# Performance work log

Hardware: AMD Instinct MI355X
Metric: run time of the kernel (lower is better)

The kernel has to match this reference:

```python
import jax, jax.numpy as jnp
import numpy as np

N_NODES = 50000
N_EDGES = 600000
D_IN = 128
D_HID = 128
D_OUT = 47
BN_EPS = 1e-5


def setup_inputs() -> dict:
    key = jax.random.key(0)
    ks = jax.random.split(key, 16)
    x = jax.random.normal(ks[0], (N_NODES, D_IN), dtype=jnp.float32)
    edge_index = jax.random.randint(ks[1], (2, N_EDGES), 0, N_NODES, dtype=jnp.int64)
    s = 0.05
    return {
        'x': x,
        'edge_index': edge_index,
        # SAGEConv layer 1: lin_l (neighbor agg, with bias), lin_r (root, no bias)
        'W1l': jax.random.normal(ks[2], (D_IN, D_HID), jnp.float32) * s,
        'b1': jnp.zeros((D_HID,), jnp.float32),
        'W1r': jax.random.normal(ks[3], (D_IN, D_HID), jnp.float32) * s,
        # layer 2
        'W2l': jax.random.normal(ks[4], (D_HID, D_HID), jnp.float32) * s,
        'b2': jnp.zeros((D_HID,), jnp.float32),
        'W2r': jax.random.normal(ks[5], (D_HID, D_HID), jnp.float32) * s,
        # layer 3
        'W3l': jax.random.normal(ks[6], (D_HID, D_OUT), jnp.float32) * s,
        'b3': jnp.zeros((D_OUT,), jnp.float32),
        'W3r': jax.random.normal(ks[7], (D_HID, D_OUT), jnp.float32) * s,
        # BatchNorm params (eval mode: running stats)
        'g1': jnp.ones((D_HID,), jnp.float32),
        'be1': jnp.zeros((D_HID,), jnp.float32),
        'm1': jax.random.normal(ks[8], (D_HID,), jnp.float32) * 0.1,
        'v1': jnp.ones((D_HID,), jnp.float32) + jax.random.uniform(ks[9], (D_HID,)) * 0.1,
        'g2': jnp.ones((D_HID,), jnp.float32),
        'be2': jnp.zeros((D_HID,), jnp.float32),
        'm2': jax.random.normal(ks[10], (D_HID,), jnp.float32) * 0.1,
        'v2': jnp.ones((D_HID,), jnp.float32) + jax.random.uniform(ks[11], (D_HID,)) * 0.1,
    }


def _sage_conv(x, src, dst, Wl, b, Wr):
    # mean aggregation of source features at destination nodes
    n = x.shape[0]
    msg = x[src]  # [E, d] gather
    agg = jax.ops.segment_sum(msg, dst, num_segments=n)
    cnt = jax.ops.segment_sum(jnp.ones((src.shape[0],), x.dtype), dst, num_segments=n)
    agg = agg / jnp.maximum(cnt, 1.0)[:, None]  # zero in-degree -> 0
    return agg @ Wl + b + x @ Wr


def _bn_eval(x, g, be, m, v):
    return (x - m) * (g * jax.lax.rsqrt(v + BN_EPS)) + be


def reference(x, edge_index, W1l, b1, W1r, W2l, b2, W2r, W3l, b3, W3r,
              g1, be1, m1, v1, g2, be2, m2, v2):
    src, dst = edge_index[0], edge_index[1]
    h = _sage_conv(x, src, dst, W1l, b1, W1r)
    h = jax.nn.relu(_bn_eval(h, g1, be1, m1, v1))  # dropout is identity in eval
    h = _sage_conv(h, src, dst, W2l, b2, W2r)
    h = jax.nn.relu(_bn_eval(h, g2, be2, m2, v2))
    return _sage_conv(h, src, dst, W3l, b3, W3r)
```

## Files before the change

### kernel.cpp

```cpp
#include <hip/hip_runtime.h>

#define NN 50000
#define NE 600000
#define D 128
#define DOUT3 47
#define ZW 64
#define BN_EPS 1e-5f
#define NPB 256
#define SB 196

typedef __attribute__((ext_vector_type(8))) short short8;
typedef __attribute__((ext_vector_type(4))) float f32x4;

__device__ inline unsigned short f2b(float f) {
  union { float f; unsigned u; } c; c.f = f;
  unsigned u = c.u;
  unsigned r = (u + 0x7FFFu + ((u >> 16) & 1u)) >> 16;
  return (unsigned short)r;
}
__device__ inline float b2f(unsigned short h) {
  union { unsigned u; float f; } c; c.u = ((unsigned)h) << 16;
  return c.f;
}

__global__ void zero_int(int* __restrict__ p, int n) {
  int i = blockIdx.x * blockDim.x + threadIdx.x;
  if (i < n) p[i] = 0;
}

__global__ __launch_bounds__(256) void prep_hist(
    const float4* __restrict__ x4, unsigned short* __restrict__ xb,
    const float* __restrict__ W1l, const float* __restrict__ W1r, unsigned short* __restrict__ Bt1,
    const float* __restrict__ W2l, const float* __restrict__ W2r, unsigned short* __restrict__ Bt2,
    const float* __restrict__ W3l, const float* __restrict__ W3r, unsigned short* __restrict__ Bt3,
    const int* __restrict__ dst, int* __restrict__ deg) {
  int b = blockIdx.x;
  int t = threadIdx.x;
  if (b < 1024) {
    long n4 = (long)NN * D / 4;
    for (long i = (long)b * 256 + t; i < n4; i += 1024L * 256) {
      float4 v = x4[i];
      uint2 p;
      p.x = (unsigned)f2b(v.x) | ((unsigned)f2b(v.y) << 16);
      p.y = (unsigned)f2b(v.z) | ((unsigned)f2b(v.w) << 16);
      *(uint2*)(xb + i * 4) = p;
    }
  } else if (b < 1280) {
    const float* Wl = (b < 1152) ? W1l : W2l;
    const float* Wr = (b < 1152) ? W1r : W2r;
    unsigned short* Bt = (b < 1152) ? Bt1 : Bt2;
    int idx = ((b < 1152) ? (b - 1024) : (b - 1152)) * 256 + t;
    int j = idx >> 8, k = idx & 255;
    float v = (k < 128) ? Wl[k * D + j] : Wr[(k - 128) * D + j];
    Bt[idx] = f2b(v);
  } else if (b < 1336) {
    int idx = (b - 1280) * 256 + t;
    if (idx < 112 * 128) {
      int j = idx >> 7, k = idx & 127;
      float v = 0.f;
      if (j < DOUT3) v = W3l[k * DOUT3 + j];
      else if (j >= 64 && j < 64 + DOUT3) v = W3r[k * DOUT3 + (j - 64)];
      Bt3[idx] = f2b(v);
    }
  } else {
    int e = (b - 1336) * 256 + t;
    if (e < NE) {
      int d = dst[e];
      d = max(0, min(NN - 1, d));
      atomicAdd(&deg[d], 1);
    }
  }
}

__global__ __launch_bounds__(NPB) void scan_local(const int* __restrict__ deg,
                                                  int* __restrict__ row_start,
                                                  int* __restrict__ partials) {
  __shared__ int s[NPB];
  int t = threadIdx.x;
  int i = blockIdx.x * NPB + t;
  int v = (i < NN) ? deg[i] : 0;
  s[t] = v;
  __syncthreads();
  for (int off = 1; off < NPB; off <<= 1) {
    int u = (t >= off) ? s[t - off] : 0;
    __syncthreads();
    s[t] += u;
    __syncthreads();
  }
  if (i < NN) row_start[i] = s[t] - v;
  if (t == NPB - 1) partials[blockIdx.x] = s[NPB - 1];
}

__global__ __launch_bounds__(NPB) void scan_add(int* __restrict__ row_start,
                                                const int* __restrict__ partials,
                                                int* __restrict__ cursor) {
  __shared__ int s[NPB];
  int t = threadIdx.x;
  int v = (t < SB) ? partials[t] : 0;
  s[t] = v;
  __syncthreads();
  for (int off = 1; off < NPB; off <<= 1) {
    int u = (t >= off) ? s[t - off] : 0;
    __syncthreads();
    s[t] += u;
    __syncthreads();
  }
  int base = s[blockIdx.x] - partials[blockIdx.x];
  int i = blockIdx.x * NPB + t;
  if (i < NN) {
    int r = row_start[i] + base;
    row_start[i] = r;
    cursor[i] = r;
  }
  if (i == 0) row_start[NN] = NE;
}

__global__ void build_kernel(const int* __restrict__ src, const int* __restrict__ dst,
                             int* __restrict__ cursor, int* __restrict__ srcs, int E) {
  int e = blockIdx.x * blockDim.x + threadIdx.x;
  if (e < E) {
    int d = dst[e];
    d = max(0, min(NN - 1, d));
    int s = src[e];
    s = max(0, min(NN - 1, s));
    int pos = atomicAdd(&cursor[d], 1);
    srcs[pos] = s;
  }
}

__global__ __launch_bounds__(256) void fused_gather_mfma(
    const unsigned short* __restrict__ feat,
    const int* __restrict__ row_start, const int* __restrict__ srcs,
    const unsigned short* __restrict__ Bt, const float* __restrict__ bias,
    const float* __restrict__ g, const float* __restrict__ be,
    const float* __restrict__ m, const float* __restrict__ v,
    unsigned short* __restrict__ outb) {
  __shared__ __align__(16) unsigned short s_a[16][136];
  int tid = threadIdx.x;
  int row0 = blockIdx.x * 16;
  int grp = tid >> 4, s = tid & 15;
  const unsigned short* fp = feat + s * 8;

  {
    int node = row0 + grp;
    int start = row_start[node], end = row_start[node + 1];
    float a[8];
#pragma unroll
    for (int i = 0; i < 8; i++) a[i] = 0.f;
    for (int base = start; base < end; base += 16) {
      int cnt = min(end - base, 16);
      int idxv = (base + s < end) ? srcs[base + s] : 0;
      int M = (cnt + 3) >> 2;
      for (int q = 0; q < M; q++) {
        int e0 = q * 4;
        int s0 = __shfl(idxv, e0 + 0, 16);
        int s1 = __shfl(idxv, e0 + 1, 16);
        int s2 = __shfl(idxv, e0 + 2, 16);
        int s3 = __shfl(idxv, e0 + 3, 16);
        float w1 = (e0 + 1 < cnt) ? 1.f : 0.f;
        float w2 = (e0 + 2 < cnt) ? 1.f : 0.f;
        float w3 = (e0 + 3 < cnt) ? 1.f : 0.f;
        short8 v0 = *(const short8*)(fp + (long)s0 * D);
        short8 v1 = *(const short8*)(fp + (long)s1 * D);
        short8 v2 = *(const short8*)(fp + (long)s2 * D);
        short8 v3 = *(const short8*)(fp + (long)s3 * D);
#pragma unroll
        for (int i = 0; i < 8; i++)
          a[i] += (b2f((unsigned short)v0[i]) + w1 * b2f((unsigned short)v1[i])) +
                  (w2 * b2f((unsigned short)v2[i]) + w3 * b2f((unsigned short)v3[i]));
      }
    }
    float iv = 1.0f / fmaxf((float)(end - start), 1.0f);
    uint4 p;
    p.x = (unsigned)f2b(a[0] * iv) | ((unsigned)f2b(a[1] * iv) << 16);
    p.y = (unsigned)f2b(a[2] * iv) | ((unsigned)f2b(a[3] * iv) << 16);
    p.z = (unsigned)f2b(a[4] * iv) | ((unsigned)f2b(a[5] * iv) << 16);
    p.w = (unsigned)f2b(a[6] * iv) | ((unsigned)f2b(a[7] * iv) << 16);
    *(uint4*)&s_a[grp][s * 8] = p;
  }

  __syncthreads();

  int lane = tid & 63, wid = tid >> 6;
  int r15 = lane & 15, hi = lane >> 4;
  f32x4 acc[2];
  acc[0] = (f32x4)(0.f);
  acc[1] = (f32x4)(0.f);

  const unsigned short* As = &s_a[r15][hi * 8];
  const unsigned short* Ax = feat + (long)(row0 + r15) * D + hi * 8;
  const unsigned short* Bp = Bt + (long)(wid * 2) * 16 * 256 + (long)r15 * 256 + hi * 8;

#pragma unroll
  for (int kf = 0; kf < 8; kf++) {
    const int kk = kf * 32;
    short8 a = (kf < 4) ? *(const short8*)(As + kk)
                        : *(const short8*)(Ax + (kk - 128));
#pragma unroll
    for (int f = 0; f < 2; f++) {
      short8 b = *(const short8*)(Bp + (long)f * 16 * 256 + kk);
      acc[f] = __builtin_amdgcn_mfma_f32_16x16x32_bf16(a, b, acc[f], 0, 0, 0);
    }
  }

#pragma unroll
  for (int f = 0; f < 2; f++) {
    int col = wid * 32 + f * 16 + r15;
    float bj = bias[col];
    float sc = g[col] * rsqrtf(v[col] + BN_EPS);
    float sh = be[col] - m[col] * sc;
#pragma unroll
    for (int r = 0; r < 4; r++) {
      int row = row0 + hi * 4 + r;
      float val = fmaxf((acc[f][r] + bj) * sc + sh, 0.f);
      outb[(long)row * D + col] = f2b(val);
    }
  }
}

__global__ __launch_bounds__(256) void trans_mfma(
    const unsigned short* __restrict__ xb, const unsigned short* __restrict__ Bt3,
    const float* __restrict__ bias, unsigned short* __restrict__ Z,
    float* __restrict__ outP, int tiles) {
  const int NF = 7;
  int wid = threadIdx.x >> 6, lane = threadIdx.x & 63;
  int tile = blockIdx.x * 4 + wid;
  if (tile >= tiles) return;
  int row0 = tile * 16;
  int r15 = lane & 15, hi = lane >> 4;

  f32x4 acc[NF];
#pragma unroll
  for (int f = 0; f < NF; f++) acc[f] = (f32x4)(0.f);

  const unsigned short* Ar = xb + (long)(row0 + r15) * D + hi * 8;
  const unsigned short* Bp = Bt3 + (long)r15 * 128 + hi * 8;

#pragma unroll
  for (int kf = 0; kf < 4; kf++) {
    const int kk = kf * 32;
    short8 a = *(const short8*)(Ar + kk);
#pragma unroll
    for (int f = 0; f < NF; f++) {
      short8 b = *(const short8*)(Bp + (long)f * 16 * 128 + kk);
      acc[f] = __builtin_amdgcn_mfma_f32_16x16x32_bf16(a, b, acc[f], 0, 0, 0);
    }
  }

#pragma unroll
  for (int f = 0; f < NF; f++) {
    int col = f * 16 + r15;
#pragma unroll
    for (int r = 0; r < 4; r++) {
      int row = row0 + hi * 4 + r;
      float val = acc[f][r];
      if (col < ZW) {
        Z[(long)row * ZW + col] = f2b(val);
      } else {
        int pc = col - 64;
        if (pc < DOUT3) outP[(long)row * DOUT3 + pc] = val + bias[pc];
      }
    }
  }
}

__global__ __launch_bounds__(256) void gather_add47(const unsigned short* __restrict__ Z,
                                                    const int* __restrict__ row_start,
                                                    const int* __restrict__ srcs,
                                                    float* __restrict__ outP) {
  int t = blockIdx.x * blockDim.x + threadIdx.x;
  int node = t >> 4;
  int s = t & 15;
  if (node >= NN) return;
  int start = row_start[node], end = row_start[node + 1];
  float a[4];
#pragma unroll
  for (int i = 0; i < 4; i++) a[i] = 0.f;
  const unsigned short* zp = Z + s * 4;
  for (int base = start; base < end; base += 16) {
    int cnt = min(end - base, 16);
    int idxv = (base + s < end) ? srcs[base + s] : 0;
    int M = (cnt + 3) >> 2;
    for (int q = 0; q < M; q++) {
      int e0 = q * 4;
      int s0 = __shfl(idxv, e0 + 0, 16);
      int s1 = __shfl(idxv, e0 + 1, 16);
      int s2 = __shfl(idxv, e0 + 2, 16);
      int s3 = __shfl(idxv, e0 + 3, 16);
      float w1 = (e0 + 1 < cnt) ? 1.f : 0.f;
      float w2 = (e0 + 2 < cnt) ? 1.f : 0.f;
      float w3 = (e0 + 3 < cnt) ? 1.f : 0.f;
      uint2 u0 = *(const uint2*)(zp + (long)s0 * ZW);
      uint2 u1 = *(const uint2*)(zp + (long)s1 * ZW);
      uint2 u2 = *(const uint2*)(zp + (long)s2 * ZW);
      uint2 u3 = *(const uint2*)(zp + (long)s3 * ZW);
      a[0] += (b2f((unsigned short)u0.x) + w1 * b2f((unsigned short)u1.x)) +
              (w2 * b2f((unsigned short)u2.x) + w3 * b2f((unsigned short)u3.x));
      a[1] += (b2f((unsigned short)(u0.x >> 16)) + w1 * b2f((unsigned short)(u1.x >> 16))) +
              (w2 * b2f((unsigned short)(u2.x >> 16)) + w3 * b2f((unsigned short)(u3.x >> 16)));
      a[2] += (b2f((unsigned short)u0.y) + w1 * b2f((unsigned short)u1.y)) +
              (w2 * b2f((unsigned short)u2.y) + w3 * b2f((unsigned short)u3.y));
      a[3] += (b2f((unsigned short)(u0.y >> 16)) + w1 * b2f((unsigned short)(u1.y >> 16))) +
              (w2 * b2f((unsigned short)(u2.y >> 16)) + w3 * b2f((unsigned short)(u3.y >> 16)));
    }
  }
  float iv = 1.0f / fmaxf((float)(end - start), 1.0f);
#pragma unroll
  for (int i = 0; i < 4; i++) {
    int c = s * 4 + i;
    if (c < DOUT3) {
      long o = (long)node * DOUT3 + c;
      outP[o] = outP[o] + a[i] * iv;
    }
  }
}

extern "C" void kernel_launch(void* const* d_in, const int* in_sizes, int n_in,
                              void* d_out, int out_size, void* d_ws, size_t ws_size,
                              hipStream_t stream) {
  const float* x = (const float*)d_in[0];
  const int* ei = (const int*)d_in[1];
  const int* src = ei;
  const int* dst = ei + NE;
  const float* W1l = (const float*)d_in[2];
  const float* b1  = (const float*)d_in[3];
  const float* W1r = (const float*)d_in[4];
  const float* W2l = (const float*)d_in[5];
  const float* b2  = (const float*)d_in[6];
  const float* W2r = (const float*)d_in[7];
  const float* W3l = (const float*)d_in[8];
  const float* b3  = (const float*)d_in[9];
  const float* W3r = (const float*)d_in[10];
  const float* g1  = (const float*)d_in[11];
  const float* be1 = (const float*)d_in[12];
  const float* m1  = (const float*)d_in[13];
  const float* v1  = (const float*)d_in[14];
  const float* g2  = (const float*)d_in[15];
  const float* be2 = (const float*)d_in[16];
  const float* m2  = (const float*)d_in[17];
  const float* v2  = (const float*)d_in[18];

  float* out = (float*)d_out;

  int* deg       = (int*)d_ws;
  int* row_start = deg + NN;
  int* cursor    = row_start + NN + 4;
  int* partials  = cursor + NN;
  int* srcs      = partials + 256;
  unsigned short* xb   = (unsigned short*)(srcs + NE);
  unsigned short* h2b  = xb + (long)NN * D;
  unsigned short* h1b  = h2b + (long)NN * D;
  unsigned short* Zb   = h1b + (long)NN * D;
  unsigned short* Bt1  = Zb + (long)NN * ZW;
  unsigned short* Bt2  = Bt1 + 128 * 256;
  unsigned short* Bt3  = Bt2 + 128 * 256;

  zero_int<<<SB, 256, 0, stream>>>(deg, NN);
  prep_hist<<<3680, 256, 0, stream>>>(
      (const float4*)x, xb, W1l, W1r, Bt1, W2l, W2r, Bt2, W3l, W3r, Bt3, dst, deg);

  scan_local<<<SB, NPB, 0, stream>>>(deg, row_start, partials);
  scan_add<<<SB, NPB, 0, stream>>>(row_start, partials, cursor);
  build_kernel<<<(NE + 255) / 256, 256, 0, stream>>>(src, dst, cursor, srcs, NE);

  int tiles = NN / 16;

  fused_gather_mfma<<<tiles, 256, 0, stream>>>(
      xb, row_start, srcs, Bt1, b1, g1, be1, m1, v1, h1b);

  fused_gather_mfma<<<tiles, 256, 0, stream>>>(
      h1b, row_start, srcs, Bt2, b2, g2, be2, m2, v2, h2b);

  trans_mfma<<<(tiles + 3) / 4, 256, 0, stream>>>(h2b, Bt3, b3, Zb, out, tiles);
  gather_add47<<<(NN * 16 + 255) / 256, 256, 0, stream>>>(Zb, row_start, srcs, out);
}
```

Before: 220.6 us.

## Fuse layer-3 transform into layer-2 kernel and unroll gathers to 8 edges

The layer-3 projection (trans_mfma) is folded into the layer-2 gather+MFMA kernel. The layer-2 activations stay in shared memory and are multiplied by Bt3 there, so h2 is never written to or read back from global memory and one launch is removed. Separately, the neighbor gathers in both the fused kernel and gather_add47 now load source indices directly, clamped to the last edge, and process 8 edges per iteration instead of shuffling 4 at a time. This gives more loads in flight per iteration, at the cost of higher register pressure and redundant index loads, since every lane in a group reads the same indices.

```diff
diff --git a/kernel.cpp b/kernel.cpp
--- a/kernel.cpp
+++ b/kernel.cpp
@@ -128,14 +128,20 @@
   }
 }
 
-__global__ __launch_bounds__(256) void fused_gather_mfma(
+template <bool TR>
+__global__ __launch_bounds__(256) void fused_layer(
     const unsigned short* __restrict__ feat,
     const int* __restrict__ row_start, const int* __restrict__ srcs,
     const unsigned short* __restrict__ Bt, const float* __restrict__ bias,
     const float* __restrict__ g, const float* __restrict__ be,
     const float* __restrict__ m, const float* __restrict__ v,
-    unsigned short* __restrict__ outb) {
+    unsigned short* __restrict__ outb,
+    const unsigned short* __restrict__ Bt3,
+    const float* __restrict__ b3,
+    unsigned short* __restrict__ Z,
+    float* __restrict__ outP) {
   __shared__ __align__(16) unsigned short s_a[16][136];
+  __shared__ __align__(16) unsigned short s_h[TR ? 16 : 1][136];
   int tid = threadIdx.x;
   int row0 = blockIdx.x * 16;
   int grp = tid >> 4, s = tid & 15;
@@ -144,30 +150,41 @@
   {
     int node = row0 + grp;
     int start = row_start[node], end = row_start[node + 1];
+    int last = end - 1;
     float a[8];
 #pragma unroll
     for (int i = 0; i < 8; i++) a[i] = 0.f;
-    for (int base = start; base < end; base += 16) {
-      int cnt = min(end - base, 16);
-      int idxv = (base + s < end) ? srcs[base + s] : 0;
-      int M = (cnt + 3) >> 2;
-      for (int q = 0; q < M; q++) {
-        int e0 = q * 4;
-        int s0 = __shfl(idxv, e0 + 0, 16);
-        int s1 = __shfl(idxv, e0 + 1, 16);
-        int s2 = __shfl(idxv, e0 + 2, 16);
-        int s3 = __shfl(idxv, e0 + 3, 16);
-        float w1 = (e0 + 1 < cnt) ? 1.f : 0.f;
-        float w2 = (e0 + 2 < cnt) ? 1.f : 0.f;
-        float w3 = (e0 + 3 < cnt) ? 1.f : 0.f;
-        short8 v0 = *(const short8*)(fp + (long)s0 * D);
-        short8 v1 = *(const short8*)(fp + (long)s1 * D);
-        short8 v2 = *(const short8*)(fp + (long)s2 * D);
-        short8 v3 = *(const short8*)(fp + (long)s3 * D);
-#pragma unroll
-        for (int i = 0; i < 8; i++)
-          a[i] += (b2f((unsigned short)v0[i]) + w1 * b2f((unsigned short)v1[i])) +
-                  (w2 * b2f((unsigned short)v2[i]) + w3 * b2f((unsigned short)v3[i]));
+    for (int e = start; e < end; e += 8) {
+      int i0 = srcs[e];
+      int i1 = srcs[min(e + 1, last)];
+      int i2 = srcs[min(e + 2, last)];
+      int i3 = srcs[min(e + 3, last)];
+      int i4 = srcs[min(e + 4, last)];
+      int i5 = srcs[min(e + 5, last)];
+      int i6 = srcs[min(e + 6, last)];
+      int i7 = srcs[min(e + 7, last)];
+      float w1 = (e + 1 < end) ? 1.f : 0.f;
+      float w2 = (e + 2 < end) ? 1.f : 0.f;
+      float w3 = (e + 3 < end) ? 1.f : 0.f;
+      float w4 = (e + 4 < end) ? 1.f : 0.f;
+      float w5 = (e + 5 < end) ? 1.f : 0.f;
+      float w6 = (e + 6 < end) ? 1.f : 0.f;
+      float w7 = (e + 7 < end) ? 1.f : 0.f;
+      short8 v0 = *(const short8*)(fp + (long)i0 * D);
+      short8 v1 = *(const short8*)(fp + (long)i1 * D);
+      short8 v2 = *(const short8*)(fp + (long)i2 * D);
+      short8 v3 = *(const short8*)(fp + (long)i3 * D);
+      short8 v4 = *(const short8*)(fp + (long)i4 * D);
+      short8 v5 = *(const short8*)(fp + (long)i5 * D);
+      short8 v6 = *(const short8*)(fp + (long)i6 * D);
+      short8 v7 = *(const short8*)(fp + (long)i7 * D);
+#pragma unroll
+      for (int i = 0; i < 8; i++) {
+        float t0 = b2f((unsigned short)v0[i]) + w1 * b2f((unsigned short)v1[i]);
+        float t1 = w2 * b2f((unsigned short)v2[i]) + w3 * b2f((unsigned short)v3[i]);
+        float t2 = w4 * b2f((unsigned short)v4[i]) + w5 * b2f((unsigned short)v5[i]);
+        float t3 = w6 * b2f((unsigned short)v6[i]) + w7 * b2f((unsigned short)v7[i]);
+        a[i] += (t0 + t1) + (t2 + t3);
       }
     }
     float iv = 1.0f / fmaxf((float)(end - start), 1.0f);
@@ -213,52 +230,41 @@
     for (int r = 0; r < 4; r++) {
       int row = row0 + hi * 4 + r;
       float val = fmaxf((acc[f][r] + bj) * sc + sh, 0.f);
-      outb[(long)row * D + col] = f2b(val);
-    }
-  }
-}
-
-__global__ __launch_bounds__(256) void trans_mfma(
-    const unsigned short* __restrict__ xb, const unsigned short* __restrict__ Bt3,
-    const float* __restrict__ bias, unsigned short* __restrict__ Z,
-    float* __restrict__ outP, int tiles) {
-  const int NF = 7;
-  int wid = threadIdx.x >> 6, lane = threadIdx.x & 63;
-  int tile = blockIdx.x * 4 + wid;
-  if (tile >= tiles) return;
-  int row0 = tile * 16;
-  int r15 = lane & 15, hi = lane >> 4;
-
-  f32x4 acc[NF];
-#pragma unroll
-  for (int f = 0; f < NF; f++) acc[f] = (f32x4)(0.f);
-
-  const unsigned short* Ar = xb + (long)(row0 + r15) * D + hi * 8;
-  const unsigned short* Bp = Bt3 + (long)r15 * 128 + hi * 8;
-
-#pragma unroll
-  for (int kf = 0; kf < 4; kf++) {
-    const int kk = kf * 32;
-    short8 a = *(const short8*)(Ar + kk);
-#pragma unroll
-    for (int f = 0; f < NF; f++) {
-      short8 b = *(const short8*)(Bp + (long)f * 16 * 128 + kk);
-      acc[f] = __builtin_amdgcn_mfma_f32_16x16x32_bf16(a, b, acc[f], 0, 0, 0);
-    }
-  }
-
-#pragma unroll
-  for (int f = 0; f < NF; f++) {
-    int col = f * 16 + r15;
-#pragma unroll
-    for (int r = 0; r < 4; r++) {
-      int row = row0 + hi * 4 + r;
-      float val = acc[f][r];
-      if (col < ZW) {
-        Z[(long)row * ZW + col] = f2b(val);
-      } else {
-        int pc = col - 64;
-        if (pc < DOUT3) outP[(long)row * DOUT3 + pc] = val + bias[pc];
+      if (TR) s_h[hi * 4 + r][col] = f2b(val);
+      else    outb[(long)row * D + col] = f2b(val);
+    }
+  }
+
+  if (TR) {
+    __syncthreads();
+
+    f32x4 acc2[2];
+    acc2[0] = (f32x4)(0.f);
+    acc2[1] = (f32x4)(0.f);
+    const unsigned short* Ah = &s_h[r15][hi * 8];
+#pragma unroll
+    for (int ff = 0; ff < 2; ff++) {
+      int fidx = wid * 2 + ff;
+      if (fidx >= 7) break;
+      const unsigned short* Bp3 = Bt3 + (long)fidx * 16 * 128 + (long)r15 * 128 + hi * 8;
+#pragma unroll
+      for (int kf = 0; kf < 4; kf++) {
+        const int kk = kf * 32;
+        short8 a = *(const short8*)(Ah + kk);
+        short8 b = *(const short8*)(Bp3 + kk);
+        acc2[ff] = __builtin_amdgcn_mfma_f32_16x16x32_bf16(a, b, acc2[ff], 0, 0, 0);
+      }
+#pragma unroll
+      for (int r = 0; r < 4; r++) {
+        int row = row0 + hi * 4 + r;
+        int col = fidx * 16 + r15;
+        float val = acc2[ff][r];
+        if (col < ZW) {
+          Z[(long)row * ZW + col] = f2b(val);
+        } else {
+          int pc = col - 64;
+          if (pc < DOUT3) outP[(long)row * DOUT3 + pc] = val + b3[pc];
+        }
       }
     }
   }
@@ -273,36 +279,51 @@
   int s = t & 15;
   if (node >= NN) return;
   int start = row_start[node], end = row_start[node + 1];
+  int last = end - 1;
   float a[4];
 #pragma unroll
   for (int i = 0; i < 4; i++) a[i] = 0.f;
   const unsigned short* zp = Z + s * 4;
-  for (int base = start; base < end; base += 16) {
-    int cnt = min(end - base, 16);
-    int idxv = (base + s < end) ? srcs[base + s] : 0;
-    int M = (cnt + 3) >> 2;
-    for (int q = 0; q < M; q++) {
-      int e0 = q * 4;
-      int s0 = __shfl(idxv, e0 + 0, 16);
-      int s1 = __shfl(idxv, e0 + 1, 16);
-      int s2 = __shfl(idxv, e0 + 2, 16);
-      int s3 = __shfl(idxv, e0 + 3, 16);
-      float w1 = (e0 + 1 < cnt) ? 1.f : 0.f;
-      float w2 = (e0 + 2 < cnt) ? 1.f : 0.f;
-      float w3 = (e0 + 3 < cnt) ? 1.f : 0.f;
-      uint2 u0 = *(const uint2*)(zp + (long)s0 * ZW);
-      uint2 u1 = *(const uint2*)(zp + (long)s1 * ZW);
-      uint2 u2 = *(const uint2*)(zp + (long)s2 * ZW);
-      uint2 u3 = *(const uint2*)(zp + (long)s3 * ZW);
-      a[0] += (b2f((unsigned short)u0.x) + w1 * b2f((unsigned short)u1.x)) +
-              (w2 * b2f((unsigned short)u2.x) + w3 * b2f((unsigned short)u3.x));
-      a[1] += (b2f((unsigned short)(u0.x >> 16)) + w1 * b2f((unsigned short)(u1.x >> 16))) +
-              (w2 * b2f((unsigned short)(u2.x >> 16)) + w3 * b2f((unsigned short)(u3.x >> 16)));
-      a[2] += (b2f((unsigned short)u0.y) + w1 * b2f((unsigned short)u1.y)) +
-              (w2 * b2f((unsigned short)u2.y) + w3 * b2f((unsigned short)u3.y));
-      a[3] += (b2f((unsigned short)(u0.y >> 16)) + w1 * b2f((unsigned short)(u1.y >> 16))) +
-              (w2 * b2f((unsigned short)(u2.y >> 16)) + w3 * b2f((unsigned short)(u3.y >> 16)));
-    }
+  for (int e = start; e < end; e += 8) {
+    int i0 = srcs[e];
+    int i1 = srcs[min(e + 1, last)];
+    int i2 = srcs[min(e + 2, last)];
+    int i3 = srcs[min(e + 3, last)];
+    int i4 = srcs[min(e + 4, last)];
+    int i5 = srcs[min(e + 5, last)];
+    int i6 = srcs[min(e + 6, last)];
+    int i7 = srcs[min(e + 7, last)];
+    float w1 = (e + 1 < end) ? 1.f : 0.f;
+    float w2 = (e + 2 < end) ? 1.f : 0.f;
+    float w3 = (e + 3 < end) ? 1.f : 0.f;
+    float w4 = (e + 4 < end) ? 1.f : 0.f;
+    float w5 = (e + 5 < end) ? 1.f : 0.f;
+    float w6 = (e + 6 < end) ? 1.f : 0.f;
+    float w7 = (e + 7 < end) ? 1.f : 0.f;
+    uint2 u0 = *(const uint2*)(zp + (long)i0 * ZW);
+    uint2 u1 = *(const uint2*)(zp + (long)i1 * ZW);
+    uint2 u2 = *(const uint2*)(zp + (long)i2 * ZW);
+    uint2 u3 = *(const uint2*)(zp + (long)i3 * ZW);
+    uint2 u4 = *(const uint2*)(zp + (long)i4 * ZW);
+    uint2 u5 = *(const uint2*)(zp + (long)i5 * ZW);
+    uint2 u6 = *(const uint2*)(zp + (long)i6 * ZW);
+    uint2 u7 = *(const uint2*)(zp + (long)i7 * ZW);
+    a[0] += (b2f((unsigned short)u0.x) + w1 * b2f((unsigned short)u1.x)) +
+            (w2 * b2f((unsigned short)u2.x) + w3 * b2f((unsigned short)u3.x)) +
+            (w4 * b2f((unsigned short)u4.x) + w5 * b2f((unsigned short)u5.x)) +
+            (w6 * b2f((unsigned short)u6.x) + w7 * b2f((unsigned short)u7.x));
+    a[1] += (b2f((unsigned short)(u0.x >> 16)) + w1 * b2f((unsigned short)(u1.x >> 16))) +
+            (w2 * b2f((unsigned short)(u2.x >> 16)) + w3 * b2f((unsigned short)(u3.x >> 16))) +
+            (w4 * b2f((unsigned short)(u4.x >> 16)) + w5 * b2f((unsigned short)(u5.x >> 16))) +
+            (w6 * b2f((unsigned short)(u6.x >> 16)) + w7 * b2f((unsigned short)(u7.x >> 16)));
+    a[2] += (b2f((unsigned short)u0.y) + w1 * b2f((unsigned short)u1.y)) +
+            (w2 * b2f((unsigned short)u2.y) + w3 * b2f((unsigned short)u3.y)) +
+            (w4 * b2f((unsigned short)u4.y) + w5 * b2f((unsigned short)u5.y)) +
+            (w6 * b2f((unsigned short)u6.y) + w7 * b2f((unsigned short)u7.y));
+    a[3] += (b2f((unsigned short)(u0.y >> 16)) + w1 * b2f((unsigned short)(u1.y >> 16))) +
+            (w2 * b2f((unsigned short)(u2.y >> 16)) + w3 * b2f((unsigned short)(u3.y >> 16))) +
+            (w4 * b2f((unsigned short)(u4.y >> 16)) + w5 * b2f((unsigned short)(u5.y >> 16))) +
+            (w6 * b2f((unsigned short)(u6.y >> 16)) + w7 * b2f((unsigned short)(u7.y >> 16)));
   }
   float iv = 1.0f / fmaxf((float)(end - start), 1.0f);
 #pragma unroll
@@ -348,8 +369,7 @@
   int* partials  = cursor + NN;
   int* srcs      = partials + 256;
   unsigned short* xb   = (unsigned short*)(srcs + NE);
-  unsigned short* h2b  = xb + (long)NN * D;
-  unsigned short* h1b  = h2b + (long)NN * D;
+  unsigned short* h1b  = xb + (long)NN * D;
   unsigned short* Zb   = h1b + (long)NN * D;
   unsigned short* Bt1  = Zb + (long)NN * ZW;
   unsigned short* Bt2  = Bt1 + 128 * 256;
@@ -365,12 +385,13 @@
 
   int tiles = NN / 16;
 
-  fused_gather_mfma<<<tiles, 256, 0, stream>>>(
-      xb, row_start, srcs, Bt1, b1, g1, be1, m1, v1, h1b);
-
-  fused_gather_mfma<<<tiles, 256, 0, stream>>>(
-      h1b, row_start, srcs, Bt2, b2, g2, be2, m2, v2, h2b);
-
-  trans_mfma<<<(tiles + 3) / 4, 256, 0, stream>>>(h2b, Bt3, b3, Zb, out, tiles);
+  fused_layer<false><<<tiles, 256, 0, stream>>>(
+      xb, row_start, srcs, Bt1, b1, g1, be1, m1, v1, h1b,
+      nullptr, nullptr, nullptr, nullptr);
+
+  fused_layer<true><<<tiles, 256, 0, stream>>>(
+      h1b, row_start, srcs, Bt2, b2, g2, be2, m2, v2, nullptr,
+      Bt3, b3, Zb, out);
+
   gather_add47<<<(NN * 16 + 255) / 256, 256, 0, stream>>>(Zb, row_start, srcs, out);
 }
```

New measurement: 216.3 us. Within noise of the previous version (-1.9%).
